# Kernel optimization log

Hardware: AMD Instinct MI355X
Metric: run time of the kernel (lower is better)

Reference implementation:

```python
import jax, jax.numpy as jnp
import numpy as np

MARGIN = 1.0
EPS = 1e-6  # F.pairwise_distance adds eps to the elementwise diff


def setup_inputs() -> dict:
    key = jax.random.key(0)
    k1, k2, k3 = jax.random.split(key, 3)
    N, D = 8192, 64
    anchor_embeddings = jax.random.normal(k1, (N, D), dtype=jnp.float32)
    positive_embeddings = jax.random.normal(k2, (N, D), dtype=jnp.float32)
    labels = jax.random.randint(k3, (N,), 0, 2, dtype=jnp.int64)
    return {
        "anchor_embeddings": anchor_embeddings,
        "positive_embeddings": positive_embeddings,
        "labels": labels,
    }


def _pairwise_dist(a, p):
    # dist[i, j] = ||(a_i + eps) - p_j||_2, matching F.pairwise_distance's
    # norm(x1 - x2 + eps). Computed via the Gram trick to avoid an [N,N,D]
    # intermediate.
    a = a + EPS
    a2 = jnp.sum(a * a, axis=-1)                      # [N]
    p2 = jnp.sum(p * p, axis=-1)                      # [N]
    sq = a2[:, None] + p2[None, :] - 2.0 * (a @ p.T)  # [N, N]
    return jnp.sqrt(jnp.maximum(sq, 1e-12))


def reference(anchor_embeddings, positive_embeddings, labels):
    N = anchor_embeddings.shape[0]
    dist = _pairwise_dist(anchor_embeddings, positive_embeddings)  # [N, N]
    pos_dist = jnp.diagonal(dist)                                  # [N], d(a_i, p_i)
    hinge = jax.nn.relu(pos_dist[:, None] - dist + MARGIN)         # [N, N]
    # pair (i, j) contributes iff labels[i] == 1 and i != j
    row_mask = (labels == 1)[:, None]
    offdiag = ~jnp.eye(N, dtype=bool)
    mask = (row_mask & offdiag).astype(hinge.dtype)
    count = jnp.sum(mask)
    total = jnp.sum(hinge * mask)
    return jnp.where(count > 0, total / jnp.maximum(count, 1.0), 0.0)
```

## Files before the change

### kernel.cpp

```cpp
#include <hip/hip_runtime.h>
#include <hip/hip_bf16.h>

#define NROWS 8192
#define DDIM 64
#define MARGIN_F 1.0f
#define EPS_F 1e-6f
#define NEG_BIG -1.0e30f


typedef __attribute__((ext_vector_type(8))) short bf16x8;
typedef __attribute__((ext_vector_type(4))) float f32x4;

static __device__ __forceinline__ unsigned short f2bf(float x) {
    __hip_bfloat16 h = __float2bfloat16(x);
    return *reinterpret_cast<unsigned short*>(&h);
}
static __device__ __forceinline__ float bf2f(unsigned short u) {
    return __uint_as_float(((unsigned)u) << 16);
}

__global__ __launch_bounds__(256) void
prep_compact_kernel(const float* __restrict__ A, const float* __restrict__ P,
                    const int* __restrict__ labels,
                    unsigned short* __restrict__ Abf, unsigned short* __restrict__ Pbf,
                    float* __restrict__ a2g, float* __restrict__ pdg,
                    float* __restrict__ p2g, float* __restrict__ hdg,
                    int* __restrict__ sel, int* __restrict__ cnt) {
    __shared__ int lab[256 * 33];
    __shared__ int scan[256];
    int t = threadIdx.x;

    if (blockIdx.x < 512) {
        int gid = blockIdx.x * 256 + t;
        int row = gid >> 4;
        int c4  = (gid & 15) * 4;
        float4 a = *(const float4*)&A[row * DDIM + c4];
        float4 p = *(const float4*)&P[row * DDIM + c4];
        a.x += EPS_F; a.y += EPS_F; a.z += EPS_F; a.w += EPS_F;
        ushort4 ab, pb;
        ab.x = f2bf(a.x); ab.y = f2bf(a.y); ab.z = f2bf(a.z); ab.w = f2bf(a.w);
        pb.x = f2bf(p.x); pb.y = f2bf(p.y); pb.z = f2bf(p.z); pb.w = f2bf(p.w);
        *(ushort4*)&Abf[row * DDIM + c4] = ab;
        *(ushort4*)&Pbf[row * DDIM + c4] = pb;
        float va2 = a.x*a.x + a.y*a.y + a.z*a.z + a.w*a.w;
        float vp2 = p.x*p.x + p.y*p.y + p.z*p.z + p.w*p.w;
        float vap = a.x*p.x + a.y*p.y + a.z*p.z + a.w*p.w;
        float vdd = bf2f(ab.x)*bf2f(pb.x) + bf2f(ab.y)*bf2f(pb.y)
                  + bf2f(ab.z)*bf2f(pb.z) + bf2f(ab.w)*bf2f(pb.w);
        #pragma unroll
        for (int off = 8; off; off >>= 1) {
            va2 += __shfl_xor(va2, off);
            vp2 += __shfl_xor(vp2, off);
            vap += __shfl_xor(vap, off);
            vdd += __shfl_xor(vdd, off);
        }
        if ((t & 15) == 0) {
            a2g[row] = va2;
            p2g[row] = vp2;
            float pd = sqrtf(fmaxf(va2 + vp2 - 2.0f * vap, 1e-12f)) + MARGIN_F;
            pdg[row] = pd;
            float sqd = fmaxf(va2 + vp2 - 2.0f * vdd, 1e-12f);
            hdg[row] = fmaxf(pd - __builtin_amdgcn_sqrtf(sqd), 0.0f);
        }
    } else {
        #pragma unroll
        for (int i = 0; i < 32; ++i) {
            int j = i * 256 + t;
            lab[(j >> 5) * 33 + (j & 31)] = labels[j];
        }
        __syncthreads();
        int lc = 0;
        #pragma unroll
        for (int i = 0; i < 32; ++i) lc += (lab[t * 33 + i] == 1) ? 1 : 0;
        scan[t] = lc;
        __syncthreads();
        for (int off = 1; off < 256; off <<= 1) {
            int v = (t >= off) ? scan[t - off] : 0;
            __syncthreads();
            if (t >= off) scan[t] += v;
            __syncthreads();
        }
        int o = scan[t] - lc;
        for (int i = 0; i < 32; ++i) {
            if (lab[t * 33 + i] == 1) sel[o++] = t * 32 + i;
        }
        if (t == 255) *cnt = scan[255];
    }
}

__global__ __launch_bounds__(256) void
main_kernel(const unsigned short* __restrict__ Abf, const unsigned short* __restrict__ Pbf,
            const float* __restrict__ a2g, const float* __restrict__ pdg,
            const float* __restrict__ p2g, const int* __restrict__ sel,
            const int* __restrict__ cnt, float* __restrict__ partial4) {
    int M = *cnt;
    int t = threadIdx.x;
    int wid  = t >> 6;
    int lane = t & 63;
    int row0 = blockIdx.y << 7;
    int col0 = blockIdx.x << 7;
    int slot = (((blockIdx.y << 6) + blockIdx.x) << 2) + wid;

    if (row0 >= M) { if (lane == 0) partial4[slot] = 0.0f; return; }

    int wm   = (wid >> 1) << 6;
    int wn   = (wid & 1) << 6;
    int lm   = lane & 15;
    int quad = lane >> 4;

    bf16x8 bg0[4], bg1[4];
    float spv[4];
    #pragma unroll
    for (int b = 0; b < 4; ++b) {
        int cj = col0 + wn + b * 16 + lm;
        const unsigned short* pb = Pbf + (size_t)cj * DDIM + quad * 8;
        bg0[b] = *(const bf16x8*)pb;
        bg1[b] = *(const bf16x8*)(pb + 32);
        spv[b] = p2g[cj];
    }

    int Lrow  = row0 + wm + lane;
    int gi    = sel[min(Lrow, M - 1)];
    float myA2 = a2g[gi];
    float myPd = (Lrow < M) ? pdg[gi] : NEG_BIG;

    bf16x8 af0[4], af1[4];
    #pragma unroll
    for (int a = 0; a < 4; ++a) {
        int gia = __shfl(gi, a * 16 + lm);
        const unsigned short* pa = Abf + (size_t)gia * DDIM + quad * 8;
        af0[a] = *(const bf16x8*)pa;
        af1[a] = *(const bf16x8*)(pa + 32);
    }

    f32x4 acc[4][4] = {};
    #pragma unroll
    for (int a = 0; a < 4; ++a)
        #pragma unroll
        for (int b = 0; b < 4; ++b)
            acc[a][b] = __builtin_amdgcn_mfma_f32_16x16x32_bf16(af0[a], bg0[b], acc[a][b], 0, 0, 0);
    #pragma unroll
    for (int a = 0; a < 4; ++a)
        #pragma unroll
        for (int b = 0; b < 4; ++b)
            acc[a][b] = __builtin_amdgcn_mfma_f32_16x16x32_bf16(af1[a], bg1[b], acc[a][b], 0, 0, 0);

    float bsum = 0.0f;
    #pragma unroll
    for (int a = 0; a < 4; ++a) {
        #pragma unroll
        for (int r = 0; r < 4; ++r) {
            int src = a * 16 + quad * 4 + r;
            float ra2 = __shfl(myA2, src);
            float rpd = __shfl(myPd, src);
            #pragma unroll
            for (int b = 0; b < 4; ++b) {
                float sq = fmaf(-2.0f, acc[a][b][r], ra2 + spv[b]);
                float h  = rpd - __builtin_amdgcn_sqrtf(sq);
                bsum += fmaxf(h, 0.0f);
            }
        }
    }

    #pragma unroll
    for (int off = 32; off; off >>= 1) bsum += __shfl_xor(bsum, off);
    if (lane == 0) partial4[slot] = bsum;
}

__global__ __launch_bounds__(256) void
finalize_kernel(const int* __restrict__ cnt, const float* __restrict__ partial4,
                const float* __restrict__ hdg, const int* __restrict__ sel,
                float* __restrict__ out) {
    __shared__ float wsum[4];
    int t = threadIdx.x;
    const float4* p4 = (const float4*)partial4;
    float s = 0.0f;
    #pragma unroll
    for (int i = 0; i < 16; ++i) {
        float4 v = p4[i * 256 + t];
        s += v.x + v.y + v.z + v.w;
    }
    int M = *cnt;
    for (int i = t; i < M; i += 256) s -= hdg[sel[i]];
    #pragma unroll
    for (int off = 32; off; off >>= 1) s += __shfl_xor(s, off);
    if ((t & 63) == 0) wsum[t >> 6] = s;
    __syncthreads();
    if (t == 0) {
        float tot = wsum[0] + wsum[1] + wsum[2] + wsum[3];
        out[0] = (M > 0) ? tot / ((float)M * (float)(NROWS - 1)) : 0.0f;
    }
}

extern "C" void kernel_launch(void* const* d_in, const int* in_sizes, int n_in,
                              void* d_out, int out_size, void* d_ws, size_t ws_size,
                              hipStream_t stream) {
    const float* A      = (const float*)d_in[0];
    const float* P      = (const float*)d_in[1];
    const int*   labels = (const int*)d_in[2];
    float* out = (float*)d_out;

    char* ws = (char*)d_ws;
    unsigned short* Abf = (unsigned short*)(ws);
    unsigned short* Pbf = (unsigned short*)(ws + (1 << 20));
    char* base = ws + (2 << 20);
    float* a2g      = (float*)(base);
    float* pdg      = (float*)(base + 32768);
    float* p2g      = (float*)(base + 65536);
    float* hdg      = (float*)(base + 98304);
    int*   sel      = (int*)(base + 131072);
    float* partial4 = (float*)(base + 163840);
    int*   cnt      = (int*)(base + 229376);

    prep_compact_kernel<<<dim3(513), dim3(256), 0, stream>>>(A, P, labels, Abf, Pbf,
                                                             a2g, pdg, p2g, hdg, sel, cnt);

    main_kernel<<<dim3(64, 64), dim3(256), 0, stream>>>(Abf, Pbf, a2g, pdg, p2g,
                                                        sel, cnt, partial4);

    finalize_kernel<<<1, dim3(256), 0, stream>>>(cnt, partial4, hdg, sel, out);
}
```

Baseline: 92.81 us.

## Use ballot-based label compaction, reorder loads, split accumulators, raise occupancy hint

New measurement: 144.0 us. 1.55x slower.

```diff
diff --git a/kernel.cpp b/kernel.cpp
--- a/kernel.cpp
+++ b/kernel.cpp
@@ -26,8 +26,6 @@
                     float* __restrict__ a2g, float* __restrict__ pdg,
                     float* __restrict__ p2g, float* __restrict__ hdg,
                     int* __restrict__ sel, int* __restrict__ cnt) {
-    __shared__ int lab[256 * 33];
-    __shared__ int scan[256];
     int t = threadIdx.x;
 
     if (blockIdx.x < 512) {
@@ -63,32 +61,47 @@
             hdg[row] = fmaxf(pd - __builtin_amdgcn_sqrtf(sqd), 0.0f);
         }
     } else {
+        __shared__ unsigned long long masks[128];
+        __shared__ int segbase[128];
+        int wid  = t >> 6;
+        int lane = t & 63;
         #pragma unroll
         for (int i = 0; i < 32; ++i) {
-            int j = i * 256 + t;
-            lab[(j >> 5) * 33 + (j & 31)] = labels[j];
+            int v = labels[i * 256 + t];
+            unsigned long long m = __ballot(v == 1);
+            if (lane == 0) masks[i * 4 + wid] = m;
         }
         __syncthreads();
-        int lc = 0;
-        #pragma unroll
-        for (int i = 0; i < 32; ++i) lc += (lab[t * 33 + i] == 1) ? 1 : 0;
-        scan[t] = lc;
+        if (wid == 0) {
+            int c0 = __popcll(masks[lane]);
+            int c1 = __popcll(masks[64 + lane]);
+            int s0 = c0, s1 = c1;
+            #pragma unroll
+            for (int off = 1; off < 64; off <<= 1) {
+                int u0 = __shfl_up(s0, off);
+                int u1 = __shfl_up(s1, off);
+                if (lane >= off) { s0 += u0; s1 += u1; }
+            }
+            int tot0 = __shfl(s0, 63);
+            segbase[lane]      = s0 - c0;
+            segbase[64 + lane] = tot0 + s1 - c1;
+            if (lane == 63) *cnt = tot0 + s1;
+        }
         __syncthreads();
-        for (int off = 1; off < 256; off <<= 1) {
-            int v = (t >= off) ? scan[t - off] : 0;
-            __syncthreads();
-            if (t >= off) scan[t] += v;
-            __syncthreads();
-        }
-        int o = scan[t] - lc;
+        unsigned long long lt = ((unsigned long long)1 << lane) - 1ull;
+        #pragma unroll
         for (int i = 0; i < 32; ++i) {
-            if (lab[t * 33 + i] == 1) sel[o++] = t * 32 + i;
-        }
-        if (t == 255) *cnt = scan[255];
-    }
-}
-
-__global__ __launch_bounds__(256) void
+            int seg = i * 4 + wid;
+            unsigned long long m = masks[seg];
+            if ((m >> lane) & 1ull) {
+                int rank = __popcll(m & lt);
+                sel[segbase[seg] + rank] = i * 256 + (wid << 6) + lane;
+            }
+        }
+    }
+}
+
+__global__ __launch_bounds__(256, 6) void
 main_kernel(const unsigned short* __restrict__ Abf, const unsigned short* __restrict__ Pbf,
             const float* __restrict__ a2g, const float* __restrict__ pdg,
             const float* __restrict__ p2g, const int* __restrict__ sel,
@@ -108,6 +121,9 @@
     int lm   = lane & 15;
     int quad = lane >> 4;
 
+    int Lrow = row0 + wm + lane;
+    int gi   = sel[min(Lrow, M - 1)];
+
     bf16x8 bg0[4], bg1[4];
     float spv[4];
     #pragma unroll
@@ -119,11 +135,6 @@
         spv[b] = p2g[cj];
     }
 
-    int Lrow  = row0 + wm + lane;
-    int gi    = sel[min(Lrow, M - 1)];
-    float myA2 = a2g[gi];
-    float myPd = (Lrow < M) ? pdg[gi] : NEG_BIG;
-
     bf16x8 af0[4], af1[4];
     #pragma unroll
     for (int a = 0; a < 4; ++a) {
@@ -133,6 +144,9 @@
         af1[a] = *(const bf16x8*)(pa + 32);
     }
 
+    float myA2 = a2g[gi];
+    float myPd = (Lrow < M) ? pdg[gi] : NEG_BIG;
+
     f32x4 acc[4][4] = {};
     #pragma unroll
     for (int a = 0; a < 4; ++a)
@@ -145,7 +159,7 @@
         for (int b = 0; b < 4; ++b)
             acc[a][b] = __builtin_amdgcn_mfma_f32_16x16x32_bf16(af1[a], bg1[b], acc[a][b], 0, 0, 0);
 
-    float bsum = 0.0f;
+    float bsum0 = 0.0f, bsum1 = 0.0f;
     #pragma unroll
     for (int a = 0; a < 4; ++a) {
         #pragma unroll
@@ -156,11 +170,12 @@
             #pragma unroll
             for (int b = 0; b < 4; ++b) {
                 float sq = fmaf(-2.0f, acc[a][b][r], ra2 + spv[b]);
-                float h  = rpd - __builtin_amdgcn_sqrtf(sq);
-                bsum += fmaxf(h, 0.0f);
+                float h  = fmaxf(rpd - __builtin_amdgcn_sqrtf(sq), 0.0f);
+                if (b & 1) bsum1 += h; else bsum0 += h;
             }
         }
     }
+    float bsum = bsum0 + bsum1;
 
     #pragma unroll
     for (int off = 32; off; off >>= 1) bsum += __shfl_xor(bsum, off);
```
